# Optimization experiments

Hardware: AMD Instinct MI355X
Metric: run time of the kernel (lower is better)

The kernel has to match this reference:

```python
import jax, jax.numpy as jnp
import numpy as np

N_NODES = 50000
N_EDGES = 800000
N_GRAPHS = 128
HEADS = 4
NEG_SLOPE = 0.2


def gat_layer(x, src, dst, W, a_src, a_dst, b, n_nodes):
    # x: [N, Fin]; W: [Fin, H*Fout]; a_src/a_dst: [H, Fout]; b: [H*Fout]
    H, Fo = a_src.shape
    h = (x @ W).reshape(n_nodes, H, Fo)                      # [N, H, Fo]
    s_src = jnp.einsum('nhf,hf->nh', h, a_src)               # [N, H]
    s_dst = jnp.einsum('nhf,hf->nh', h, a_dst)               # [N, H]
    e = jax.nn.leaky_relu(s_src[src] + s_dst[dst], NEG_SLOPE)  # [E, H]
    # segment softmax over destination nodes
    emax = jax.ops.segment_max(e, dst, num_segments=n_nodes)
    ex = jnp.exp(e - emax[dst])
    denom = jax.ops.segment_sum(ex, dst, num_segments=n_nodes)
    alpha = ex / (denom[dst] + 1e-16)                        # [E, H]
    msg = h[src] * alpha[:, :, None]                         # [E, H, Fo]
    out = jax.ops.segment_sum(msg, dst, num_segments=n_nodes)
    return out.reshape(n_nodes, H * Fo) + b


def setup_inputs() -> dict:
    key = jax.random.key(0)
    ks = jax.random.split(key, 16)
    x = jax.random.normal(ks[0], (N_NODES, 128), dtype=jnp.float32)
    edge_index = jax.random.randint(ks[1], (2, N_EDGES), 0, N_NODES, dtype=jnp.int64 if jax.config.jax_enable_x64 else jnp.int32)
    batch_index = jnp.sort(jax.random.randint(ks[2], (N_NODES,), 0, N_GRAPHS))
    s = 0.1
    # layer 0: in=128 -> H=4, Fo=32  => hidden 128
    W0 = jax.random.normal(ks[3], (128, HEADS * 32), jnp.float32) * s
    a_src0 = jax.random.normal(ks[4], (HEADS, 32), jnp.float32) * s
    a_dst0 = jax.random.normal(ks[5], (HEADS, 32), jnp.float32) * s
    b0 = jnp.zeros((HEADS * 32,), jnp.float32)
    # layer 1: in=128 -> H=4, Fo=64 => hidden 256
    W1 = jax.random.normal(ks[6], (128, HEADS * 64), jnp.float32) * s
    a_src1 = jax.random.normal(ks[7], (HEADS, 64), jnp.float32) * s
    a_dst1 = jax.random.normal(ks[8], (HEADS, 64), jnp.float32) * s
    b1 = jnp.zeros((HEADS * 64,), jnp.float32)
    # layer 2: in=256 -> H=4, Fo=64 => hidden 256
    W2 = jax.random.normal(ks[9], (256, HEADS * 64), jnp.float32) * s
    a_src2 = jax.random.normal(ks[10], (HEADS, 64), jnp.float32) * s
    a_dst2 = jax.random.normal(ks[11], (HEADS, 64), jnp.float32) * s
    b2 = jnp.zeros((HEADS * 64,), jnp.float32)
    # readout linear: 512 -> 10
    Wout = jax.random.normal(ks[12], (512, 10), jnp.float32) * s
    bout = jnp.zeros((10,), jnp.float32)
    return dict(x=x, edge_index=edge_index, batch_index=batch_index,
                W0=W0, a_src0=a_src0, a_dst0=a_dst0, b0=b0,
                W1=W1, a_src1=a_src1, a_dst1=a_dst1, b1=b1,
                W2=W2, a_src2=a_src2, a_dst2=a_dst2, b2=b2,
                Wout=Wout, bout=bout)


def reference(x, edge_index, batch_index,
              W0, a_src0, a_dst0, b0,
              W1, a_src1, a_dst1, b1,
              W2, a_src2, a_dst2, b2,
              Wout, bout):
    n = x.shape[0]
    loops = jnp.arange(n, dtype=edge_index.dtype)
    src = jnp.concatenate([edge_index[0], loops])  # PyG add_self_loops
    dst = jnp.concatenate([edge_index[1], loops])
    h = jax.nn.relu(gat_layer(x, src, dst, W0, a_src0, a_dst0, b0, n))
    h = jax.nn.relu(gat_layer(h, src, dst, W1, a_src1, a_dst1, b1, n))
    h = jax.nn.relu(gat_layer(h, src, dst, W2, a_src2, a_dst2, b2, n))
    # global mean / max pool per graph
    ssum = jax.ops.segment_sum(h, batch_index, num_segments=N_GRAPHS)
    cnt = jax.ops.segment_sum(jnp.ones((n, 1), h.dtype), batch_index, num_segments=N_GRAPHS)
    gmean = ssum / jnp.maximum(cnt, 1.0)
    gmax = jax.ops.segment_max(h, batch_index, num_segments=N_GRAPHS)
    pooled = jnp.concatenate([gmean, gmax], axis=1)  # [G, 512]
    return pooled @ Wout + bout
```

## Files before the change

kernel.cpp:

```cpp
#include <hip/hip_runtime.h>
#include <cfloat>

#define N_NODES 50000
#define N_EDGES 800000
#define E_TOT   850000
#define NG      128
#define NH      4
#define CHUNK   782

typedef float f4 __attribute__((ext_vector_type(4)));
typedef float v4f __attribute__((ext_vector_type(4)));
typedef _Float16 h2v __attribute__((ext_vector_type(2)));
typedef _Float16 h8v __attribute__((ext_vector_type(8)));

__global__ void count_dst_k(const int* __restrict__ ei, int* __restrict__ cnt) {
    int e = blockIdx.x * blockDim.x + threadIdx.x;
    if (e >= E_TOT) return;
    int d = (e < N_EDGES) ? ei[N_EDGES + e] : (e - N_EDGES);
    atomicAdd(&cnt[d], 1);
}

__global__ void scan_sums_k(const int* __restrict__ cnt, int* __restrict__ bsum) {
    int b = blockIdx.x;
    int start = b * CHUNK, end2 = min(start + CHUNK, N_NODES);
    int lane = threadIdx.x & 63, wv = threadIdx.x >> 6;
    int s = 0;
    for (int i = start + threadIdx.x; i < end2; i += 256) s += cnt[i];
    #pragma unroll
    for (int off = 32; off; off >>= 1) s += __shfl_xor(s, off);
    __shared__ int ws[4];
    if (lane == 0) ws[wv] = s;
    __syncthreads();
    if (threadIdx.x == 0) bsum[b] = ws[0] + ws[1] + ws[2] + ws[3];
}

__global__ void scan_off_k(int* __restrict__ bsum, int* __restrict__ row_ptr) {
    int lane = threadIdx.x;
    int v = bsum[lane];
    int s = v;
    #pragma unroll
    for (int off = 1; off < 64; off <<= 1) {
        int t = __shfl_up(s, off);
        if (lane >= off) s += t;
    }
    bsum[lane] = s - v;
    if (lane == 63) row_ptr[N_NODES] = s;
}

__global__ void scan_write_k(const int* __restrict__ cnt, const int* __restrict__ bsum,
                             int* __restrict__ row_ptr, int* __restrict__ cursor) {
    int b = blockIdx.x;
    int start = b * CHUNK, end2 = min(start + CHUNK, N_NODES);
    __shared__ int wsum[4];
    __shared__ int carry_sh;
    int lane = threadIdx.x & 63, wv = threadIdx.x >> 6;
    if (threadIdx.x == 0) carry_sh = bsum[b];
    __syncthreads();
    for (int base = start; base < end2; base += 256) {
        int i = base + threadIdx.x;
        int v = (i < end2) ? cnt[i] : 0;
        int s = v;
        #pragma unroll
        for (int off = 1; off < 64; off <<= 1) {
            int t = __shfl_up(s, off);
            if (lane >= off) s += t;
        }
        if (lane == 63) wsum[wv] = s;
        __syncthreads();
        int woff = 0;
        #pragma unroll
        for (int k = 0; k < 4; ++k) if (k < wv) woff += wsum[k];
        int carry = carry_sh;
        if (i < end2) { int rp = carry + woff + s - v; row_ptr[i] = rp; cursor[i] = rp; }
        __syncthreads();
        if (threadIdx.x == 0) carry_sh = carry + wsum[0] + wsum[1] + wsum[2] + wsum[3];
        __syncthreads();
    }
}

__global__ void fill_k(const int* __restrict__ ei, int* __restrict__ cursor,
                       int* __restrict__ col) {
    int e = blockIdx.x * blockDim.x + threadIdx.x;
    if (e >= E_TOT) return;
    int s, d;
    if (e < N_EDGES) { s = ei[e]; d = ei[N_EDGES + e]; }
    else { s = e - N_EDGES; d = s; }
    int slot = atomicAdd(&cursor[d], 1);
    col[slot] = s;
}

template<int K, int NOUT>
__global__ void pack_w_k(const float* __restrict__ W, _Float16* __restrict__ Wp) {
    constexpr int total = (NOUT / 16) * (K / 32) * 64;
    int t = blockIdx.x * blockDim.x + threadIdx.x;
    if (t >= total) return;
    int lane = t & 63;
    int rest = t >> 6;
    int ks = rest % (K / 32);
    int n  = rest / (K / 32);
    int colW = n * 16 + (lane & 15);
    int krow = ks * 32 + (lane >> 4) * 8;
    h8v v;
    #pragma unroll
    for (int j = 0; j < 8; ++j) v[j] = (_Float16)W[(size_t)(krow + j) * NOUT + colW];
    *(h8v*)(Wp + (size_t)t * 8) = v;
}

template<int K, int NOUT, typename XT>
__global__ __launch_bounds__(256) void gemm_k(const XT* __restrict__ x,
                                              const _Float16* __restrict__ Wp,
                                              const float* __restrict__ asrc,
                                              const float* __restrict__ adst,
                                              _Float16* __restrict__ outh,
                                              float* __restrict__ ssrc,
                                              float* __restrict__ sdst) {
    constexpr int SLICE = NOUT / 8;
    constexpr int Fo  = NOUT / NH;
    constexpr int FoT = Fo / 16;
    constexpr int KS  = K / 32;
    constexpr int NT  = NOUT / 16;
    constexpr int LK  = K + 8;
    __shared__ __align__(16) _Float16 xs[64 * LK];
    int row0 = blockIdx.x * 64;
    for (int seg = threadIdx.x; seg < 64 * K / 8; seg += 256) {
        int r = seg / (K / 8);
        int c = (seg % (K / 8)) * 8;
        h8v v = {};
        if (row0 + r < N_NODES) {
            if constexpr (sizeof(XT) == 2) {
                v = *(const h8v*)((const _Float16*)x + (size_t)(row0 + r) * K + c);
            } else {
                const float* xp = (const float*)x + (size_t)(row0 + r) * K + c;
                float4 a = *(const float4*)xp;
                float4 b = *(const float4*)(xp + 4);
                v[0] = (_Float16)a.x; v[1] = (_Float16)a.y;
                v[2] = (_Float16)a.z; v[3] = (_Float16)a.w;
                v[4] = (_Float16)b.x; v[5] = (_Float16)b.y;
                v[6] = (_Float16)b.z; v[7] = (_Float16)b.w;
            }
        }
        *(h8v*)(xs + r * LK + c) = v;
    }
    __syncthreads();
    int wv = threadIdx.x >> 6, lane = threadIdx.x & 63;
    int quad = lane >> 4, colL = lane & 15;
    int r0 = row0 + wv * 16;
    h8v afr[KS];
    #pragma unroll
    for (int ks = 0; ks < KS; ++ks)
        afr[ks] = *(const h8v*)(xs + (wv * 16 + colL) * LK + ks * 32 + quad * 8);
    const h8v* bp = (const h8v*)Wp;
    float psa[4] = {0.f, 0.f, 0.f, 0.f}, pda[4] = {0.f, 0.f, 0.f, 0.f};
    #pragma unroll
    for (int t = 0; t < NT; ++t) {
        v4f acc = {};
        #pragma unroll
        for (int ks = 0; ks < KS; ++ks) {
            h8v bfr = bp[(size_t)(t * KS + ks) * 64 + lane];
            acc = __builtin_amdgcn_mfma_f32_16x16x32_f16(afr[ks], bfr, acc, 0, 0, 0);
        }
        int n0 = t * 16;
        int col = n0 + colL;
        float as_ = asrc[col], ad_ = adst[col];
        int sl = n0 / SLICE;
        int so = col % SLICE;
        _Float16* op = outh + (size_t)sl * N_NODES * SLICE + so;
        #pragma unroll
        for (int reg = 0; reg < 4; ++reg) {
            int row = r0 + quad * 4 + reg;
            float cv = acc[reg];
            if (row < N_NODES) op[(size_t)row * SLICE] = (_Float16)cv;
            float ps = cv * as_, pd = cv * ad_;
            #pragma unroll
            for (int off = 1; off < 16; off <<= 1) {
                ps += __shfl_xor(ps, off);
                pd += __shfl_xor(pd, off);
            }
            psa[reg] += ps; pda[reg] += pd;
        }
        if ((t & (FoT - 1)) == (FoT - 1)) {
            int hd = t / FoT;
            if (colL == 0) {
                #pragma unroll
                for (int reg = 0; reg < 4; ++reg) {
                    int row = r0 + quad * 4 + reg;
                    if (row < N_NODES) {
                        ssrc[row * NH + hd] = psa[reg];
                        sdst[row * NH + hd] = pda[reg];
                    }
                }
            }
            #pragma unroll
            for (int reg = 0; reg < 4; ++reg) { psa[reg] = 0.f; pda[reg] = 0.f; }
        }
    }
}

__global__ __launch_bounds__(256) void alpha_k(const float* __restrict__ ssrc,
                                               const float* __restrict__ sdst,
                                               const int* __restrict__ row_ptr,
                                               const int* __restrict__ col,
                                               float* __restrict__ alpha) {
    int wv = threadIdx.x >> 6, lane = threadIdx.x & 63;
    int v = blockIdx.x * 4 + wv;
    if (v >= N_NODES) return;
    int hd = lane >> 4, lg = lane & 15;
    int beg = row_ptr[v], cnt = row_ptr[v + 1] - beg;
    float sdv = sdst[v * NH + hd];
    float* pl = alpha + (size_t)hd * E_TOT + beg;

    if (cnt <= 128) {
        float er[8];
        float m = -FLT_MAX;
        #pragma unroll
        for (int i = 0; i < 8; ++i) {
            int j = lg + i * 16;
            if (j < cnt) {
                int u = col[beg + j];
                float e = ssrc[u * NH + hd] + sdv;
                e = (e > 0.f) ? e : 0.2f * e;
                er[i] = e;
                m = fmaxf(m, e);
            }
        }
        #pragma unroll
        for (int off = 1; off < 16; off <<= 1) m = fmaxf(m, __shfl_xor(m, off));
        float den = 0.f;
        #pragma unroll
        for (int i = 0; i < 8; ++i) {
            int j = lg + i * 16;
            if (j < cnt) { float w = __expf(er[i] - m); er[i] = w; den += w; }
        }
        #pragma unroll
        for (int off = 1; off < 16; off <<= 1) den += __shfl_xor(den, off);
        float inv = 1.f / (den + 1e-16f);
        #pragma unroll
        for (int i = 0; i < 8; ++i) {
            int j = lg + i * 16;
            if (j < cnt) pl[j] = er[i] * inv;
        }
    } else {
        float m = -FLT_MAX;
        for (int j = lg; j < cnt; j += 16) {
            int u = col[beg + j];
            float e = ssrc[u * NH + hd] + sdv;
            e = (e > 0.f) ? e : 0.2f * e;
            m = fmaxf(m, e);
        }
        #pragma unroll
        for (int off = 1; off < 16; off <<= 1) m = fmaxf(m, __shfl_xor(m, off));
        float den = 0.f;
        for (int j = lg; j < cnt; j += 16) {
            int u = col[beg + j];
            float e = ssrc[u * NH + hd] + sdv;
            e = (e > 0.f) ? e : 0.2f * e;
            den += __expf(e - m);
        }
        #pragma unroll
        for (int off = 1; off < 16; off <<= 1) den += __shfl_xor(den, off);
        float inv = 1.f / (den + 1e-16f);
        for (int j = lg; j < cnt; j += 16) {
            int u = col[beg + j];
            float e = ssrc[u * NH + hd] + sdv;
            e = (e > 0.f) ? e : 0.2f * e;
            pl[j] = __expf(e - m) * inv;
        }
    }
}

template<int HFo, int SLICE, int LPN>
__global__ __launch_bounds__(256) void agg3_k(const _Float16* __restrict__ hh,
                                              const float* __restrict__ alpha,
                                              const int* __restrict__ row_ptr,
                                              const int* __restrict__ col,
                                              const float* __restrict__ bias,
                                              _Float16* __restrict__ outH) {
    constexpr int Fo   = HFo / NH;
    constexpr int NPW  = 64 / LPN;
    constexpr int NPB  = 4 * NPW;
    constexpr int CAPW = NPW * 32;
    __shared__ int   colS[4][CAPW];
    __shared__ float awS[4][CAPW];
    int s = blockIdx.x & 7;
    int g = blockIdx.x >> 3;
    int wv = threadIdx.x >> 6, lane = threadIdx.x & 63;
    int sub = lane / LPN, lq = lane % LPN;
    int vFirst = g * NPB + wv * NPW;
    if (vFirst >= N_NODES) return;
    int vCount = min(NPW, N_NODES - vFirst);
    int hd = (s * SLICE) / Fo;
    const float* ap = alpha + (size_t)hd * E_TOT;
    int begW = row_ptr[vFirst];
    int endW = row_ptr[vFirst + vCount];
    int len = endW - begW;
    bool active = sub < vCount;
    int v = vFirst + sub;
    int beg = 0, cnt = 0;
    if (active) { beg = row_ptr[v]; cnt = row_ptr[v + 1] - beg; }
    const _Float16* hp = hh + (size_t)s * N_NODES * SLICE + lq * 8;
    float acc[8] = {};

    if (len <= CAPW) {
        for (int t = lane; t < len; t += 64) {
            colS[wv][t] = col[begW + t];
            awS[wv][t]  = ap[begW + t];
        }
        __builtin_amdgcn_wave_barrier();
        int off = beg - begW;
        int j = 0;
        for (; j + 8 <= cnt; j += 8) {
            int u[8]; float w[8]; h8v hv[8];
            #pragma unroll
            for (int i = 0; i < 8; ++i) { u[i] = colS[wv][off + j + i]; w[i] = awS[wv][off + j + i]; }
            #pragma unroll
            for (int i = 0; i < 8; ++i) hv[i] = *(const h8v*)(hp + (size_t)u[i] * SLICE);
            #pragma unroll
            for (int i = 0; i < 8; ++i)
                #pragma unroll
                for (int c = 0; c < 8; ++c) acc[c] += w[i] * (float)hv[i][c];
        }
        for (; j < cnt; ++j) {
            int u = colS[wv][off + j];
            float w = awS[wv][off + j];
            h8v hv = *(const h8v*)(hp + (size_t)u * SLICE);
            #pragma unroll
            for (int c = 0; c < 8; ++c) acc[c] += w * (float)hv[c];
        }
    } else {
        const int*   cp = col + beg;
        const float* app = ap + beg;
        for (int j = 0; j < cnt; ++j) {
            int u = cp[j];
            float w = app[j];
            h8v hv = *(const h8v*)(hp + (size_t)u * SLICE);
            #pragma unroll
            for (int c = 0; c < 8; ++c) acc[c] += w * (float)hv[c];
        }
    }
    if (active) {
        int f0 = s * SLICE + lq * 8;
        h8v res;
        #pragma unroll
        for (int c = 0; c < 8; ++c) res[c] = (_Float16)fmaxf(acc[c] + bias[f0 + c], 0.f);
        *(h8v*)(outH + (size_t)v * HFo + f0) = res;
    }
}

__global__ void pool_k(const _Float16* __restrict__ h, const int* __restrict__ batch,
                       float* __restrict__ gsum, float* __restrict__ gmax) {
    int f = threadIdx.x;
    int n0 = blockIdx.x * 32;
    int nend = min(n0 + 32, N_NODES);
    int cur = -1;
    float sa = 0.f, ma = 0.f;
    for (int n = n0; n < nend; ++n) {
        int g = batch[n];
        float val = (float)h[(size_t)n * 256 + f];
        if (g != cur) {
            if (cur >= 0) {
                atomicAdd(&gsum[cur * 256 + f], sa);
                atomicMax((int*)&gmax[cur * 256 + f], __float_as_int(ma));
            }
            cur = g; sa = 0.f; ma = 0.f;
        }
        sa += val;
        ma = fmaxf(ma, val);
    }
    if (cur >= 0) {
        atomicAdd(&gsum[cur * 256 + f], sa);
        atomicMax((int*)&gmax[cur * 256 + f], __float_as_int(ma));
    }
}

__global__ void gcnt_k(const int* __restrict__ batch, int* __restrict__ gcnt) {
    int g = threadIdx.x;
    if (g >= NG) return;
    int lo = 0, hi = N_NODES;
    while (lo < hi) { int mid = (lo + hi) >> 1; if (batch[mid] < g) lo = mid + 1; else hi = mid; }
    int b0 = lo;
    lo = 0; hi = N_NODES;
    while (lo < hi) { int mid = (lo + hi) >> 1; if (batch[mid] < g + 1) lo = mid + 1; else hi = mid; }
    gcnt[g] = lo - b0;
}

__global__ void readout_k(const float* __restrict__ gsum, const float* __restrict__ gmax,
                          const int* __restrict__ gcnt, const float* __restrict__ Wout,
                          const float* __restrict__ bout, float* __restrict__ out) {
    int g = blockIdx.x, lane = threadIdx.x;
    float inv = 1.f / fmaxf((float)gcnt[g], 1.f);
    float acc[10];
    #pragma unroll
    for (int j = 0; j < 10; ++j) acc[j] = 0.f;
    for (int f = lane; f < 512; f += 64) {
        float p = (f < 256) ? gsum[g * 256 + f] * inv : gmax[g * 256 + (f - 256)];
        #pragma unroll
        for (int j = 0; j < 10; ++j) acc[j] += p * Wout[f * 10 + j];
    }
    #pragma unroll
    for (int j = 0; j < 10; ++j) {
        float a = acc[j];
        #pragma unroll
        for (int off = 32; off; off >>= 1) a += __shfl_xor(a, off);
        if (lane == 0) out[g * 10 + j] = a + bout[j];
    }
}

extern "C" void kernel_launch(void* const* d_in, const int* in_sizes, int n_in,
                              void* d_out, int out_size, void* d_ws, size_t ws_size,
                              hipStream_t stream) {
    const float* x    = (const float*)d_in[0];
    const int*   ei   = (const int*)d_in[1];
    const int*   batch= (const int*)d_in[2];
    const float* W0   = (const float*)d_in[3];
    const float* as0  = (const float*)d_in[4];
    const float* ad0  = (const float*)d_in[5];
    const float* b0   = (const float*)d_in[6];
    const float* W1   = (const float*)d_in[7];
    const float* as1  = (const float*)d_in[8];
    const float* ad1  = (const float*)d_in[9];
    const float* b1   = (const float*)d_in[10];
    const float* W2   = (const float*)d_in[11];
    const float* as2  = (const float*)d_in[12];
    const float* ad2  = (const float*)d_in[13];
    const float* b2   = (const float*)d_in[14];
    const float* Wout = (const float*)d_in[15];
    const float* bout = (const float*)d_in[16];
    float* out = (float*)d_out;

    char* ws = (char*)d_ws;
    size_t o = 0;
    auto take = [&](size_t bytes) { size_t r = o; o += (bytes + 255) & ~(size_t)255; return r; };
    size_t cnt_o  = take((size_t)N_NODES * 4);
    size_t gsum_o = take((size_t)NG * 256 * 4);
    size_t gmax_o = take((size_t)NG * 256 * 4);
    size_t gcnt_o = take((size_t)NG * 4);
    size_t zero_bytes = o;
    size_t rp_o   = take((size_t)(N_NODES + 1) * 4);
    size_t cur_o  = take((size_t)N_NODES * 4);
    size_t bsum_o = take((size_t)64 * 4);
    size_t col_o  = take((size_t)E_TOT * 4);
    size_t ssrc_o = take((size_t)N_NODES * NH * 4);
    size_t sdst_o = take((size_t)N_NODES * NH * 4);
    size_t alp_o  = take((size_t)NH * E_TOT * 4);
    size_t hh_o   = take((size_t)N_NODES * 256 * 2);
    size_t bufH_o = take((size_t)N_NODES * 256 * 2);
    size_t wp0_o  = take((size_t)128 * 128 * 2);
    size_t wp1_o  = take((size_t)128 * 256 * 2);
    size_t wp2_o  = take((size_t)256 * 256 * 2);

    int*      cnt    = (int*)(ws + cnt_o);
    float*    gsum   = (float*)(ws + gsum_o);
    float*    gmax   = (float*)(ws + gmax_o);
    int*      gcnt   = (int*)(ws + gcnt_o);
    int*      row_ptr= (int*)(ws + rp_o);
    int*      cursor = (int*)(ws + cur_o);
    int*      bsum   = (int*)(ws + bsum_o);
    int*      col    = (int*)(ws + col_o);
    float*    ssrc   = (float*)(ws + ssrc_o);
    float*    sdst   = (float*)(ws + sdst_o);
    float*    alpha  = (float*)(ws + alp_o);
    _Float16* hH     = (_Float16*)(ws + hh_o);
    _Float16* bufH   = (_Float16*)(ws + bufH_o);
    _Float16* Wp0    = (_Float16*)(ws + wp0_o);
    _Float16* Wp1    = (_Float16*)(ws + wp1_o);
    _Float16* Wp2    = (_Float16*)(ws + wp2_o);

    (void)hipMemsetAsync(ws, 0, zero_bytes, stream);

    count_dst_k<<<(E_TOT + 255) / 256, 256, 0, stream>>>(ei, cnt);
    scan_sums_k<<<64, 256, 0, stream>>>(cnt, bsum);
    scan_off_k<<<1, 64, 0, stream>>>(bsum, row_ptr);
    scan_write_k<<<64, 256, 0, stream>>>(cnt, bsum, row_ptr, cursor);
    fill_k<<<(E_TOT + 255) / 256, 256, 0, stream>>>(ei, cursor, col);

    pack_w_k<128, 128><<<8, 256, 0, stream>>>(W0, Wp0);
    pack_w_k<128, 256><<<16, 256, 0, stream>>>(W1, Wp1);
    pack_w_k<256, 256><<<32, 256, 0, stream>>>(W2, Wp2);

    int gemm_grid  = (N_NODES + 63) / 64;
    int alpha_grid = (N_NODES + 3) / 4;
    int agg128_grid = 8 * ((N_NODES + 127) / 128);
    int agg256_grid = 8 * ((N_NODES + 63) / 64);

    gemm_k<128, 128, float><<<gemm_grid, 256, 0, stream>>>(x, Wp0, as0, ad0, hH, ssrc, sdst);
    alpha_k<<<alpha_grid, 256, 0, stream>>>(ssrc, sdst, row_ptr, col, alpha);
    agg3_k<128, 16, 2><<<agg128_grid, 256, 0, stream>>>(hH, alpha, row_ptr, col, b0, bufH);

    gemm_k<128, 256, _Float16><<<gemm_grid, 256, 0, stream>>>(bufH, Wp1, as1, ad1, hH, ssrc, sdst);
    alpha_k<<<alpha_grid, 256, 0, stream>>>(ssrc, sdst, row_ptr, col, alpha);
    agg3_k<256, 32, 4><<<agg256_grid, 256, 0, stream>>>(hH, alpha, row_ptr, col, b1, bufH);

    gemm_k<256, 256, _Float16><<<gemm_grid, 256, 0, stream>>>(bufH, Wp2, as2, ad2, hH, ssrc, sdst);
    alpha_k<<<alpha_grid, 256, 0, stream>>>(ssrc, sdst, row_ptr, col, alpha);
    agg3_k<256, 32, 4><<<agg256_grid, 256, 0, stream>>>(hH, alpha, row_ptr, col, b2, bufH);

    pool_k<<<(N_NODES + 31) / 32, 256, 0, stream>>>(bufH, batch, gsum, gmax);
    gcnt_k<<<1, 128, 0, stream>>>(batch, gcnt);
    readout_k<<<NG, 64, 0, stream>>>(gsum, gmax, gcnt, Wout, bout, out);
}
```

Measured before the change: 533.2 us.

## Fold attention vectors into extra GEMM column tile for score computation

```diff
diff --git a/kernel.cpp b/kernel.cpp
--- a/kernel.cpp
+++ b/kernel.cpp
@@ -10,7 +10,6 @@
 
 typedef float f4 __attribute__((ext_vector_type(4)));
 typedef float v4f __attribute__((ext_vector_type(4)));
-typedef _Float16 h2v __attribute__((ext_vector_type(2)));
 typedef _Float16 h8v __attribute__((ext_vector_type(8)));
 
 __global__ void count_dst_k(const int* __restrict__ ei, int* __restrict__ cnt) {
@@ -106,17 +105,39 @@
     *(h8v*)(Wp + (size_t)t * 8) = v;
 }
 
+template<int K, int NOUT>
+__global__ void pack_a_k(const float* __restrict__ W, const float* __restrict__ asrc,
+                         const float* __restrict__ adst, _Float16* __restrict__ Wp) {
+    constexpr int KS = K / 32;
+    constexpr int NT = NOUT / 16;
+    constexpr int Fo = NOUT / NH;
+    int t = blockIdx.x * blockDim.x + threadIdx.x;
+    if (t >= KS * 64) return;
+    int ks = t >> 6, lane = t & 63;
+    int colL = lane & 15;
+    int krow = ks * 32 + ((lane >> 4) & 3) * 8;
+    h8v v = {};
+    if (colL < 8) {
+        int hd = colL & 3;
+        const float* av = (colL < 4) ? asrc : adst;
+        #pragma unroll
+        for (int j = 0; j < 8; ++j) {
+            float s = 0.f;
+            const float* wr = W + (size_t)(krow + j) * NOUT + hd * Fo;
+            for (int f = 0; f < Fo; ++f) s += wr[f] * av[hd * Fo + f];
+            v[j] = (_Float16)s;
+        }
+    }
+    *(h8v*)(Wp + (size_t)((NT * KS + ks) * 64 + lane) * 8) = v;
+}
+
 template<int K, int NOUT, typename XT>
 __global__ __launch_bounds__(256) void gemm_k(const XT* __restrict__ x,
                                               const _Float16* __restrict__ Wp,
-                                              const float* __restrict__ asrc,
-                                              const float* __restrict__ adst,
                                               _Float16* __restrict__ outh,
                                               float* __restrict__ ssrc,
                                               float* __restrict__ sdst) {
     constexpr int SLICE = NOUT / 8;
-    constexpr int Fo  = NOUT / NH;
-    constexpr int FoT = Fo / 16;
     constexpr int KS  = K / 32;
     constexpr int NT  = NOUT / 16;
     constexpr int LK  = K + 8;
@@ -150,48 +171,33 @@
     for (int ks = 0; ks < KS; ++ks)
         afr[ks] = *(const h8v*)(xs + (wv * 16 + colL) * LK + ks * 32 + quad * 8);
     const h8v* bp = (const h8v*)Wp;
-    float psa[4] = {0.f, 0.f, 0.f, 0.f}, pda[4] = {0.f, 0.f, 0.f, 0.f};
-    #pragma unroll
-    for (int t = 0; t < NT; ++t) {
+    #pragma unroll
+    for (int t = 0; t <= NT; ++t) {
         v4f acc = {};
         #pragma unroll
         for (int ks = 0; ks < KS; ++ks) {
             h8v bfr = bp[(size_t)(t * KS + ks) * 64 + lane];
             acc = __builtin_amdgcn_mfma_f32_16x16x32_f16(afr[ks], bfr, acc, 0, 0, 0);
         }
-        int n0 = t * 16;
-        int col = n0 + colL;
-        float as_ = asrc[col], ad_ = adst[col];
-        int sl = n0 / SLICE;
-        int so = col % SLICE;
-        _Float16* op = outh + (size_t)sl * N_NODES * SLICE + so;
-        #pragma unroll
-        for (int reg = 0; reg < 4; ++reg) {
-            int row = r0 + quad * 4 + reg;
-            float cv = acc[reg];
-            if (row < N_NODES) op[(size_t)row * SLICE] = (_Float16)cv;
-            float ps = cv * as_, pd = cv * ad_;
-            #pragma unroll
-            for (int off = 1; off < 16; off <<= 1) {
-                ps += __shfl_xor(ps, off);
-                pd += __shfl_xor(pd, off);
+        if (t < NT) {
+            int n0 = t * 16;
+            int col = n0 + colL;
+            int sl = n0 / SLICE;
+            int so = col % SLICE;
+            _Float16* op = outh + (size_t)sl * N_NODES * SLICE + so;
+            #pragma unroll
+            for (int reg = 0; reg < 4; ++reg) {
+                int row = r0 + quad * 4 + reg;
+                if (row < N_NODES) op[(size_t)row * SLICE] = (_Float16)acc[reg];
             }
-            psa[reg] += ps; pda[reg] += pd;
-        }
-        if ((t & (FoT - 1)) == (FoT - 1)) {
-            int hd = t / FoT;
-            if (colL == 0) {
-                #pragma unroll
-                for (int reg = 0; reg < 4; ++reg) {
-                    int row = r0 + quad * 4 + reg;
-                    if (row < N_NODES) {
-                        ssrc[row * NH + hd] = psa[reg];
-                        sdst[row * NH + hd] = pda[reg];
-                    }
-                }
+        } else if (colL < 8) {
+            int hd = colL & 3;
+            float* sp = (colL < 4) ? ssrc : sdst;
+            #pragma unroll
+            for (int reg = 0; reg < 4; ++reg) {
+                int row = r0 + quad * 4 + reg;
+                if (row < N_NODES) sp[row * NH + hd] = acc[reg];
             }
-            #pragma unroll
-            for (int reg = 0; reg < 4; ++reg) { psa[reg] = 0.f; pda[reg] = 0.f; }
         }
     }
 }
@@ -444,9 +450,9 @@
     size_t alp_o  = take((size_t)NH * E_TOT * 4);
     size_t hh_o   = take((size_t)N_NODES * 256 * 2);
     size_t bufH_o = take((size_t)N_NODES * 256 * 2);
-    size_t wp0_o  = take((size_t)128 * 128 * 2);
-    size_t wp1_o  = take((size_t)128 * 256 * 2);
-    size_t wp2_o  = take((size_t)256 * 256 * 2);
+    size_t wp0_o  = take((size_t)(8 + 1) * 4 * 64 * 8 * 2);
+    size_t wp1_o  = take((size_t)(16 + 1) * 4 * 64 * 8 * 2);
+    size_t wp2_o  = take((size_t)(16 + 1) * 8 * 64 * 8 * 2);
 
     int*      cnt    = (int*)(ws + cnt_o);
     float*    gsum   = (float*)(ws + gsum_o);
@@ -476,21 +482,24 @@
     pack_w_k<128, 128><<<8, 256, 0, stream>>>(W0, Wp0);
     pack_w_k<128, 256><<<16, 256, 0, stream>>>(W1, Wp1);
     pack_w_k<256, 256><<<32, 256, 0, stream>>>(W2, Wp2);
+    pack_a_k<128, 128><<<1, 256, 0, stream>>>(W0, as0, ad0, Wp0);
+    pack_a_k<128, 256><<<1, 256, 0, stream>>>(W1, as1, ad1, Wp1);
+    pack_a_k<256, 256><<<2, 256, 0, stream>>>(W2, as2, ad2, Wp2);
 
     int gemm_grid  = (N_NODES + 63) / 64;
     int alpha_grid = (N_NODES + 3) / 4;
     int agg128_grid = 8 * ((N_NODES + 127) / 128);
     int agg256_grid = 8 * ((N_NODES + 63) / 64);
 
-    gemm_k<128, 128, float><<<gemm_grid, 256, 0, stream>>>(x, Wp0, as0, ad0, hH, ssrc, sdst);
+    gemm_k<128, 128, float><<<gemm_grid, 256, 0, stream>>>(x, Wp0, hH, ssrc, sdst);
     alpha_k<<<alpha_grid, 256, 0, stream>>>(ssrc, sdst, row_ptr, col, alpha);
     agg3_k<128, 16, 2><<<agg128_grid, 256, 0, stream>>>(hH, alpha, row_ptr, col, b0, bufH);
 
-    gemm_k<128, 256, _Float16><<<gemm_grid, 256, 0, stream>>>(bufH, Wp1, as1, ad1, hH, ssrc, sdst);
+    gemm_k<128, 256, _Float16><<<gemm_grid, 256, 0, stream>>>(bufH, Wp1, hH, ssrc, sdst);
     alpha_k<<<alpha_grid, 256, 0, stream>>>(ssrc, sdst, row_ptr, col, alpha);
     agg3_k<256, 32, 4><<<agg256_grid, 256, 0, stream>>>(hH, alpha, row_ptr, col, b1, bufH);
 
-    gemm_k<256, 256, _Float16><<<gemm_grid, 256, 0, stream>>>(bufH, Wp2, as2, ad2, hH, ssrc, sdst);
+    gemm_k<256, 256, _Float16><<<gemm_grid, 256, 0, stream>>>(bufH, Wp2, hH, ssrc, sdst);
     alpha_k<<<alpha_grid, 256, 0, stream>>>(ssrc, sdst, row_ptr, col, alpha);
     agg3_k<256, 32, 4><<<agg256_grid, 256, 0, stream>>>(hH, alpha, row_ptr, col, b2, bufH);
 
```

New measurement: 525.8 us. About the same (-1.4%).
